# Performance work log

Measured on AMD Instinct MI355X. Metric: run time of the kernel, lower is better.

## Reference

```python
import jax, jax.numpy as jnp
import numpy as np

DIM = 128
WS = 7          # window size
NH = 4          # num heads
N = WS * WS     # tokens per window = 49
GRID = 56       # 224/4 token grid -> 8x8 = 64 windows per image
NUM_WIN = (GRID // WS) ** 2  # 64
IMG_B = 64
SCALE = (DIM // NH) ** -0.5


def _relative_position_index():
    coords = np.stack(np.meshgrid(np.arange(WS), np.arange(WS), indexing='ij'))  # (2,WS,WS)
    flat = coords.reshape(2, -1)                         # (2, N)
    rel = flat[:, :, None] - flat[:, None, :]            # (2, N, N)
    rel = rel.transpose(1, 2, 0).astype(np.int32)        # (N, N, 2)
    rel[:, :, 0] += WS - 1
    rel[:, :, 1] += WS - 1
    rel[:, :, 0] *= 2 * WS - 1
    return jnp.asarray(rel.sum(-1))                      # (N, N) int32


def _shift_mask():
    # Swin shifted-window attention mask: shift = WS // 2, off-group pairs get -100.
    shift = WS // 2
    img = np.zeros((GRID, GRID), dtype=np.int32)
    cnt = 0
    segs = (slice(0, -WS), slice(-WS, -shift), slice(-shift, None))
    for hs in segs:
        for ws_ in segs:
            img[hs, ws_] = cnt
            cnt += 1
    # window partition -> (NUM_WIN, N)
    w = img.reshape(GRID // WS, WS, GRID // WS, WS).transpose(0, 2, 1, 3).reshape(NUM_WIN, N)
    diff = w[:, :, None] - w[:, None, :]
    return jnp.asarray(np.where(diff != 0, -100.0, 0.0).astype(np.float32))  # (NUM_WIN, N, N)


def setup_inputs() -> dict:
    key = jax.random.key(0)
    ks = jax.random.split(key, 6)
    B = IMG_B * NUM_WIN  # 4096
    x = jax.random.normal(ks[0], (B, N, DIM), dtype=jnp.float32)
    qkv_w = jax.random.normal(ks[1], (3 * DIM, DIM), dtype=jnp.float32) * (DIM ** -0.5)
    qkv_b = jnp.zeros((3 * DIM,), dtype=jnp.float32)
    proj_w = jax.random.normal(ks[2], (DIM, DIM), dtype=jnp.float32) * (DIM ** -0.5)
    proj_b = jnp.zeros((DIM,), dtype=jnp.float32)
    rel_bias_table = jax.random.normal(ks[3], ((2 * WS - 1) ** 2, NH), dtype=jnp.float32) * 0.02
    return {
        'x': x,
        'mask': _shift_mask(),
        'qkv_w': qkv_w,
        'qkv_b': qkv_b,
        'proj_w': proj_w,
        'proj_b': proj_b,
        'rel_bias_table': rel_bias_table,
        'rel_index': _relative_position_index(),
    }


def reference(x, mask, qkv_w, qkv_b, proj_w, proj_b, rel_bias_table, rel_index):
    B, n, C = x.shape
    hd = C // NH
    qkv = (x @ qkv_w.T + qkv_b).reshape(B, n, 3, NH, hd)
    q = qkv[:, :, 0].transpose(0, 2, 1, 3) * SCALE   # (B, H, N, hd)
    k = qkv[:, :, 1].transpose(0, 2, 1, 3)
    v = qkv[:, :, 2].transpose(0, 2, 1, 3)
    attn = jnp.einsum('bhnd,bhmd->bhnm', q, k)       # (B, H, N, N)
    bias = rel_bias_table[rel_index.reshape(-1)].reshape(n, n, NH).transpose(2, 0, 1)
    attn = attn + bias[None]
    nW = mask.shape[0]
    attn = attn.reshape(B // nW, nW, NH, n, n) + mask[None, :, None]
    attn = jax.nn.softmax(attn.reshape(B, NH, n, n), axis=-1)
    out = jnp.einsum('bhnm,bhmd->bhnd', attn, v).transpose(0, 2, 1, 3).reshape(B, n, C)
    return out @ proj_w.T + proj_b
```

## Files before the change

### kernel.cpp

```cpp
#include <hip/hip_runtime.h>


#define NTOK  49
#define DIMC  128
#define NBLK  4096
#define SCALE 0.17677669529663687f

typedef __attribute__((ext_vector_type(8))) short bf16x8;
typedef __attribute__((ext_vector_type(4))) float f32x4;

#define WS_QKVW 0
#define WS_PROJW 49152
#define WS_BIAS  65536
#define WS_TOTAL 81920

#define XS_OFF 0
#define XS_STRIDE 136
#define PS_OFF 6664
#define PS_STRIDE 72
#define QS_OFF 10192
#define QS_STRIDE 40
#define KS_OFF 20432
#define VT_OFF 30672
#define VT_STRIDE 72
#define SMEM_TOT 39888

__device__ __forceinline__ unsigned int pkbf2(float f0, float f1) {
    union { float f; unsigned int i; } a, b; a.f = f0; b.f = f1;
    return __builtin_amdgcn_perm(b.i + 0x8000u, a.i + 0x8000u, 0x07060302u);
}
__device__ __forceinline__ unsigned short f2b_r(float f) {
    union { float f; unsigned int i; } v; v.f = f;
    return (unsigned short)((v.i + 0x8000u) >> 16);
}
__device__ __forceinline__ float b2f_lo(unsigned int u) {
    union { unsigned int i; float f; } v; v.i = u << 16; return v.f;
}
__device__ __forceinline__ float b2f_hi(unsigned int u) {
    union { unsigned int i; float f; } v; v.i = u & 0xFFFF0000u; return v.f;
}

__device__ __forceinline__ int seg3(int c) { return (c < 49) ? 0 : ((c < 53) ? 1 : 2); }

__global__ __launch_bounds__(256)
void prep(const float* __restrict__ qkv_w, const float* __restrict__ proj_w,
          const float* __restrict__ bias_t, const int* __restrict__ rel_idx,
          unsigned short* __restrict__ ws)
{
    int idx = blockIdx.x * 256 + threadIdx.x;
    if (idx < 8192) {
        int base = idx * 8;
        const float* sp = (base < 49152) ? (qkv_w + base) : (proj_w + (base - 49152));
        float sc = (base < 16384) ? SCALE : 1.0f;
        float4 a = *(const float4*)sp;
        float4 b = *(const float4*)(sp + 4);
        uint4 u;
        u.x = pkbf2(a.x * sc, a.y * sc);
        u.y = pkbf2(a.z * sc, a.w * sc);
        u.z = pkbf2(b.x * sc, b.y * sc);
        u.w = pkbf2(b.z * sc, b.w * sc);
        *(uint4*)(ws + base) = u;
    } else {
        int i = idx - 8192;
        int reg = i & 3, lane = (i >> 2) & 63, nt = (i >> 8) & 3,
            mt = (i >> 10) & 3, h = (i >> 12) & 3;
        int row = mt * 16 + (lane >> 4) * 4 + reg;
        int col = nt * 16 + (lane & 15);
        float v = 0.f;
        if (row < NTOK && col < NTOK)
            v = bias_t[rel_idx[row * NTOK + col] * 4 + h];
        ws[WS_BIAS + i] = f2b_r(v);
    }
}

__global__ __launch_bounds__(256, 2)
void win_attn(const float* __restrict__ x,
              const float* __restrict__ qkv_b,
              const float* __restrict__ proj_b,
              const unsigned short* __restrict__ ws,
              float* __restrict__ out)
{
    __shared__ unsigned short smem[SMEM_TOT];
    const int b    = blockIdx.x;
    const int w    = b & 63;
    const int tid  = threadIdx.x;
    const int wv   = tid >> 6;
    const int lane = tid & 63;
    const int qg   = lane >> 4;
    const int l15  = lane & 15;

    {
        const float4* xg = (const float4*)(x + (size_t)b * (NTOK * DIMC));
        for (int i = tid; i < NTOK * DIMC / 4; i += 256) {
            float4 v = xg[i];
            int row = i >> 5, col = (i & 31) * 4;
            uint2 u; u.x = pkbf2(v.x, v.y); u.y = pkbf2(v.z, v.w);
            *(uint2*)(smem + XS_OFF + row * XS_STRIDE + col) = u;
        }
    }
    __syncthreads();

    bf16x8 af[4][4];
    #pragma unroll
    for (int mt = 0; mt < 4; mt++) {
        int ar = mt * 16 + l15; if (ar > 48) ar = 48;
        #pragma unroll
        for (int ks_ = 0; ks_ < 4; ks_++)
            af[mt][ks_] = *(const bf16x8*)(smem + XS_OFF + ar * XS_STRIDE + ks_ * 32 + qg * 8);
    }

    {
        const unsigned short* qw = ws + WS_QKVW;
        #pragma unroll
        for (int part = 0; part < 3; part++) {
            #pragma unroll
            for (int half = 0; half < 2; half++) {
                const int jt = part * 8 + wv * 2 + half;
                const int j  = jt * 16 + l15;
                bf16x8 bf[4];
                #pragma unroll
                for (int ks_ = 0; ks_ < 4; ks_++)
                    bf[ks_] = *(const bf16x8*)(qw + j * DIMC + ks_ * 32 + qg * 8);
                const float bias = (part == 0) ? qkv_b[j] * SCALE : qkv_b[j];
                #pragma unroll
                for (int mt = 0; mt < 4; mt++) {
                    f32x4 acc = { bias, bias, bias, bias };
                    #pragma unroll
                    for (int ks_ = 0; ks_ < 4; ks_++)
                        acc = __builtin_amdgcn_mfma_f32_16x16x32_bf16(af[mt][ks_], bf[ks_], acc, 0, 0, 0);
                    const int d = half * 16 + l15;
                    if (part == 0) {
                        #pragma unroll
                        for (int r = 0; r < 4; r++) {
                            int row = mt * 16 + qg * 4 + r;
                            smem[QS_OFF + (wv * 64 + row) * QS_STRIDE + d] = f2b_r(acc[r]);
                        }
                    } else if (part == 1) {
                        #pragma unroll
                        for (int r = 0; r < 4; r++) {
                            int row = mt * 16 + qg * 4 + r;
                            smem[KS_OFF + (wv * 64 + row) * QS_STRIDE + d] = f2b_r(acc[r]);
                        }
                    } else {
                        uint2 u; u.x = pkbf2(acc[0], acc[1]); u.y = pkbf2(acc[2], acc[3]);
                        *(uint2*)(smem + VT_OFF + (wv * 32 + d) * VT_STRIDE + mt * 16 + qg * 4) = u;
                    }
                }
            }
        }
    }
    __syncthreads();

    const int wy = w >> 3, wx = w & 7;
    int g_row[4], g_col[4]; bool vcol[4];
    #pragma unroll
    for (int r = 0; r < 4; r++) {
        int t = wv * 16 + qg * 4 + r;
        int ty = (t * 9363) >> 16, tx = t - ty * 7;
        g_row[r] = seg3(wy * 7 + ty) * 3 + seg3(wx * 7 + tx);
    }
    #pragma unroll
    for (int nt = 0; nt < 4; nt++) {
        int t = nt * 16 + l15;
        int ty = (t * 9363) >> 16, tx = t - ty * 7;
        g_col[nt] = seg3(wy * 7 + ty) * 3 + seg3(wx * 7 + tx);
        vcol[nt] = t < NTOK;
    }

    const int r0 = wv * 16;
    for (int h = 0; h < 4; h++) {
        bf16x8 aq = *(const bf16x8*)(smem + QS_OFF + (h * 64 + r0 + l15) * QS_STRIDE + qg * 8);
        float s[4][4];
        #pragma unroll
        for (int nt = 0; nt < 4; nt++) {
            bf16x8 bk = *(const bf16x8*)(smem + KS_OFF + (h * 64 + nt * 16 + l15) * QS_STRIDE + qg * 8);
            f32x4 z = { 0.f, 0.f, 0.f, 0.f };
            f32x4 c = __builtin_amdgcn_mfma_f32_16x16x32_bf16(aq, bk, z, 0, 0, 0);
            uint2 bb = *(const uint2*)(ws + WS_BIAS + (((h * 4 + wv) * 4 + nt) * 64 + lane) * 4);
            float bv[4] = { b2f_lo(bb.x), b2f_hi(bb.x), b2f_lo(bb.y), b2f_hi(bb.y) };
            #pragma unroll
            for (int r = 0; r < 4; r++) {
                float v = c[r] + bv[r];
                v += (g_row[r] == g_col[nt]) ? 0.f : -100.f;
                s[nt][r] = vcol[nt] ? v : -1e30f;
            }
        }
        float p[4][4];
        #pragma unroll
        for (int r = 0; r < 4; r++) {
            float mx = fmaxf(fmaxf(s[0][r], s[1][r]), fmaxf(s[2][r], s[3][r]));
            mx = fmaxf(mx, __shfl_xor(mx, 1));
            mx = fmaxf(mx, __shfl_xor(mx, 2));
            mx = fmaxf(mx, __shfl_xor(mx, 4));
            mx = fmaxf(mx, __shfl_xor(mx, 8));
            float sum = 0.f;
            #pragma unroll
            for (int nt = 0; nt < 4; nt++) {
                float e = vcol[nt] ? __expf(s[nt][r] - mx) : 0.f;
                p[nt][r] = e; sum += e;
            }
            sum += __shfl_xor(sum, 1);
            sum += __shfl_xor(sum, 2);
            sum += __shfl_xor(sum, 4);
            sum += __shfl_xor(sum, 8);
            float inv = 1.f / sum;
            #pragma unroll
            for (int nt = 0; nt < 4; nt++) p[nt][r] *= inv;
        }
        #pragma unroll
        for (int nt = 0; nt < 4; nt++)
            #pragma unroll
            for (int r = 0; r < 4; r++) {
                int row = r0 + qg * 4 + r;
                if (row < NTOK)
                    smem[PS_OFF + row * PS_STRIDE + nt * 16 + l15] = f2b_r(p[nt][r]);
            }
        int ar2 = r0 + l15; if (ar2 > 48) ar2 = 48;
        f32x4 accO[2] = { { 0.f, 0.f, 0.f, 0.f }, { 0.f, 0.f, 0.f, 0.f } };
        #pragma unroll
        for (int ks2 = 0; ks2 < 2; ks2++) {
            bf16x8 ap = *(const bf16x8*)(smem + PS_OFF + ar2 * PS_STRIDE + ks2 * 32 + qg * 8);
            #pragma unroll
            for (int nt2 = 0; nt2 < 2; nt2++) {
                bf16x8 bv = *(const bf16x8*)(smem + VT_OFF + (h * 32 + nt2 * 16 + l15) * VT_STRIDE + ks2 * 32 + qg * 8);
                accO[nt2] = __builtin_amdgcn_mfma_f32_16x16x32_bf16(ap, bv, accO[nt2], 0, 0, 0);
            }
        }
        #pragma unroll
        for (int nt2 = 0; nt2 < 2; nt2++)
            #pragma unroll
            for (int r = 0; r < 4; r++) {
                int row = r0 + qg * 4 + r;
                if (row < NTOK)
                    smem[XS_OFF + row * XS_STRIDE + h * 32 + nt2 * 16 + l15] = f2b_r(accO[nt2][r]);
            }
    }
    __syncthreads();

    {
        #pragma unroll
        for (int mt = 0; mt < 4; mt++) {
            int ar = mt * 16 + l15; if (ar > 48) ar = 48;
            #pragma unroll
            for (int ks_ = 0; ks_ < 4; ks_++)
                af[mt][ks_] = *(const bf16x8*)(smem + XS_OFF + ar * XS_STRIDE + ks_ * 32 + qg * 8);
        }
        const unsigned short* pw = ws + WS_PROJW;
        float* ob = out + (size_t)b * (NTOK * DIMC);
        #pragma unroll
        for (int half = 0; half < 2; half++) {
            const int j = (wv * 2 + half) * 16 + l15;
            bf16x8 bf[4];
            #pragma unroll
            for (int ks_ = 0; ks_ < 4; ks_++)
                bf[ks_] = *(const bf16x8*)(pw + j * DIMC + ks_ * 32 + qg * 8);
            const float pb = proj_b[j];
            #pragma unroll
            for (int mt = 0; mt < 4; mt++) {
                f32x4 acc = { pb, pb, pb, pb };
                #pragma unroll
                for (int ks_ = 0; ks_ < 4; ks_++)
                    acc = __builtin_amdgcn_mfma_f32_16x16x32_bf16(af[mt][ks_], bf[ks_], acc, 0, 0, 0);
                #pragma unroll
                for (int r = 0; r < 4; r++) {
                    int row = mt * 16 + qg * 4 + r;
                    if (row < NTOK) ob[row * DIMC + j] = acc[r];
                }
            }
        }
    }
}

extern "C" void kernel_launch(void* const* d_in, const int* in_sizes, int n_in,
                              void* d_out, int out_size, void* d_ws, size_t ws_size,
                              hipStream_t stream) {
    const float* x      = (const float*)d_in[0];
    const float* qkv_w  = (const float*)d_in[2];
    const float* qkv_b  = (const float*)d_in[3];
    const float* proj_w = (const float*)d_in[4];
    const float* proj_b = (const float*)d_in[5];
    const float* bias_t = (const float*)d_in[6];
    const int*   relidx = (const int*)d_in[7];
    float*       outp   = (float*)d_out;
    unsigned short* ws  = (unsigned short*)d_ws;

    prep<<<96, 256, 0, stream>>>(qkv_w, proj_w, bias_t, relidx, ws);
    win_attn<<<NBLK, 256, 0, stream>>>(x, qkv_b, proj_b, ws, outp);
}
```

Baseline: 299.2 us.

## Use 512-thread blocks with head-split attention, exp2 softmax, and compact LDS

```diff
diff --git a/kernel.cpp b/kernel.cpp
--- a/kernel.cpp
+++ b/kernel.cpp
@@ -5,6 +5,8 @@
 #define DIMC  128
 #define NBLK  4096
 #define SCALE 0.17677669529663687f
+#define LOG2E 1.4426950408889634f
+#define NMASK -144.26950408889634f
 
 typedef __attribute__((ext_vector_type(8))) short bf16x8;
 typedef __attribute__((ext_vector_type(4))) float f32x4;
@@ -14,16 +16,17 @@
 #define WS_BIAS  65536
 #define WS_TOTAL 81920
 
-#define XS_OFF 0
+#define PS_OFF    0
+#define PS_G      3528
+#define PS_STRIDE 72
 #define XS_STRIDE 136
-#define PS_OFF 6664
-#define PS_STRIDE 72
-#define QS_OFF 10192
+#define QS_OFF    7056
+#define QS_HB     2080
 #define QS_STRIDE 40
-#define KS_OFF 20432
-#define VT_OFF 30672
+#define KS_OFF    15376
+#define VT_OFF    23696
 #define VT_STRIDE 72
-#define SMEM_TOT 39888
+#define SMEM_TOT  32912
 
 __device__ __forceinline__ unsigned int pkbf2(float f0, float f1) {
     union { float f; unsigned int i; } a, b; a.f = f0; b.f = f1;
@@ -38,6 +41,9 @@
 }
 __device__ __forceinline__ float b2f_hi(unsigned int u) {
     union { unsigned int i; float f; } v; v.i = u & 0xFFFF0000u; return v.f;
+}
+__device__ __forceinline__ float exp2_hw(float x) {
+    float r; asm("v_exp_f32 %0, %1" : "=v"(r) : "v"(x)); return r;
 }
 
 __device__ __forceinline__ int seg3(int c) { return (c < 49) ? 0 : ((c < 53) ? 1 : 2); }
@@ -51,7 +57,7 @@
     if (idx < 8192) {
         int base = idx * 8;
         const float* sp = (base < 49152) ? (qkv_w + base) : (proj_w + (base - 49152));
-        float sc = (base < 16384) ? SCALE : 1.0f;
+        float sc = (base < 16384) ? (SCALE * LOG2E) : 1.0f;
         float4 a = *(const float4*)sp;
         float4 b = *(const float4*)(sp + 4);
         uint4 u;
@@ -68,12 +74,12 @@
         int col = nt * 16 + (lane & 15);
         float v = 0.f;
         if (row < NTOK && col < NTOK)
-            v = bias_t[rel_idx[row * NTOK + col] * 4 + h];
+            v = bias_t[rel_idx[row * NTOK + col] * 4 + h] * LOG2E;
         ws[WS_BIAS + i] = f2b_r(v);
     }
 }
 
-__global__ __launch_bounds__(256, 2)
+__global__ __launch_bounds__(512, 4)
 void win_attn(const float* __restrict__ x,
               const float* __restrict__ qkv_b,
               const float* __restrict__ proj_b,
@@ -91,11 +97,22 @@
 
     {
         const float4* xg = (const float4*)(x + (size_t)b * (NTOK * DIMC));
-        for (int i = tid; i < NTOK * DIMC / 4; i += 256) {
-            float4 v = xg[i];
-            int row = i >> 5, col = (i & 31) * 4;
-            uint2 u; u.x = pkbf2(v.x, v.y); u.y = pkbf2(v.z, v.w);
-            *(uint2*)(smem + XS_OFF + row * XS_STRIDE + col) = u;
+        #pragma unroll
+        for (int it = 0; it < 4; it++) {
+            int i = tid + it * 512;
+            if (i < NTOK * DIMC / 4) {
+                float4 v = xg[i];
+                int row = i >> 5, col = (i & 31) * 4;
+                uint2 u; u.x = pkbf2(v.x, v.y); u.y = pkbf2(v.z, v.w);
+                *(uint2*)(smem + PS_OFF + row * XS_STRIDE + col) = u;
+            }
+        }
+        if (tid < 384) {
+            int hz = tid / 96;
+            int rem = tid - hz * 96;
+            int rowz = NTOK + (rem >> 5);
+            int dz = rem & 31;
+            smem[KS_OFF + hz * QS_HB + rowz * QS_STRIDE + dz] = 0;
         }
     }
     __syncthreads();
@@ -106,89 +123,96 @@
         int ar = mt * 16 + l15; if (ar > 48) ar = 48;
         #pragma unroll
         for (int ks_ = 0; ks_ < 4; ks_++)
-            af[mt][ks_] = *(const bf16x8*)(smem + XS_OFF + ar * XS_STRIDE + ks_ * 32 + qg * 8);
+            af[mt][ks_] = *(const bf16x8*)(smem + PS_OFF + ar * XS_STRIDE + ks_ * 32 + qg * 8);
     }
 
     {
         const unsigned short* qw = ws + WS_QKVW;
-        #pragma unroll
-        for (int part = 0; part < 3; part++) {
-            #pragma unroll
-            for (int half = 0; half < 2; half++) {
-                const int jt = part * 8 + wv * 2 + half;
-                const int j  = jt * 16 + l15;
-                bf16x8 bf[4];
+        const int h2 = wv >> 1;
+        const int dh = (wv & 1) * 16 + l15;
+        #pragma unroll
+        for (int pp = 0; pp < 3; pp++) {
+            const int j = (pp * 8 + wv) * 16 + l15;
+            bf16x8 bfr[4];
+            #pragma unroll
+            for (int ks_ = 0; ks_ < 4; ks_++)
+                bfr[ks_] = *(const bf16x8*)(qw + j * DIMC + ks_ * 32 + qg * 8);
+            const float bias = (pp == 0) ? qkv_b[j] * (SCALE * LOG2E) : qkv_b[j];
+            #pragma unroll
+            for (int mt = 0; mt < 4; mt++) {
+                f32x4 acc = { bias, bias, bias, bias };
                 #pragma unroll
                 for (int ks_ = 0; ks_ < 4; ks_++)
-                    bf[ks_] = *(const bf16x8*)(qw + j * DIMC + ks_ * 32 + qg * 8);
-                const float bias = (part == 0) ? qkv_b[j] * SCALE : qkv_b[j];
-                #pragma unroll
-                for (int mt = 0; mt < 4; mt++) {
-                    f32x4 acc = { bias, bias, bias, bias };
+                    acc = __builtin_amdgcn_mfma_f32_16x16x32_bf16(af[mt][ks_], bfr[ks_], acc, 0, 0, 0);
+                if (pp == 0) {
                     #pragma unroll
-                    for (int ks_ = 0; ks_ < 4; ks_++)
-                        acc = __builtin_amdgcn_mfma_f32_16x16x32_bf16(af[mt][ks_], bf[ks_], acc, 0, 0, 0);
-                    const int d = half * 16 + l15;
-                    if (part == 0) {
-                        #pragma unroll
-                        for (int r = 0; r < 4; r++) {
-                            int row = mt * 16 + qg * 4 + r;
-                            smem[QS_OFF + (wv * 64 + row) * QS_STRIDE + d] = f2b_r(acc[r]);
-                        }
-                    } else if (part == 1) {
-                        #pragma unroll
-                        for (int r = 0; r < 4; r++) {
-                            int row = mt * 16 + qg * 4 + r;
-                            smem[KS_OFF + (wv * 64 + row) * QS_STRIDE + d] = f2b_r(acc[r]);
-                        }
-                    } else {
-                        uint2 u; u.x = pkbf2(acc[0], acc[1]); u.y = pkbf2(acc[2], acc[3]);
-                        *(uint2*)(smem + VT_OFF + (wv * 32 + d) * VT_STRIDE + mt * 16 + qg * 4) = u;
+                    for (int r = 0; r < 4; r++) {
+                        int row = mt * 16 + qg * 4 + r;
+                        if (row < NTOK)
+                            smem[QS_OFF + h2 * QS_HB + row * QS_STRIDE + dh] = f2b_r(acc[r]);
                     }
+                } else if (pp == 1) {
+                    #pragma unroll
+                    for (int r = 0; r < 4; r++) {
+                        int row = mt * 16 + qg * 4 + r;
+                        if (row < NTOK)
+                            smem[KS_OFF + h2 * QS_HB + row * QS_STRIDE + dh] = f2b_r(acc[r]);
+                    }
+                } else {
+                    uint2 u; u.x = pkbf2(acc[0], acc[1]); u.y = pkbf2(acc[2], acc[3]);
+                    *(uint2*)(smem + VT_OFF + (h2 * 32 + dh) * VT_STRIDE + mt * 16 + qg * 4) = u;
                 }
             }
         }
     }
     __syncthreads();
 
+    const int g  = wv >> 2;
+    const int st = wv & 3;
+    const int r0 = st * 16;
     const int wy = w >> 3, wx = w & 7;
-    int g_row[4], g_col[4]; bool vcol[4];
+    float mreg[4][4];
+    {
+        int grow[4];
+        #pragma unroll
+        for (int r = 0; r < 4; r++) {
+            int t = r0 + qg * 4 + r;
+            int ty = (t * 9363) >> 16, tx = t - ty * 7;
+            grow[r] = seg3(wy * 7 + ty) * 3 + seg3(wx * 7 + tx);
+        }
+        #pragma unroll
+        for (int nt = 0; nt < 4; nt++) {
+            int t = nt * 16 + l15;
+            int ty = (t * 9363) >> 16, tx = t - ty * 7;
+            int gcol = seg3(wy * 7 + ty) * 3 + seg3(wx * 7 + tx);
+            bool vc = t < NTOK;
+            #pragma unroll
+            for (int r = 0; r < 4; r++)
+                mreg[nt][r] = !vc ? -1e30f : ((grow[r] == gcol) ? 0.f : NMASK);
+        }
+    }
+    int ar2 = r0 + l15; if (ar2 > 48) ar2 = 48;
+
     #pragma unroll
-    for (int r = 0; r < 4; r++) {
-        int t = wv * 16 + qg * 4 + r;
-        int ty = (t * 9363) >> 16, tx = t - ty * 7;
-        g_row[r] = seg3(wy * 7 + ty) * 3 + seg3(wx * 7 + tx);
-    }
-    #pragma unroll
-    for (int nt = 0; nt < 4; nt++) {
-        int t = nt * 16 + l15;
-        int ty = (t * 9363) >> 16, tx = t - ty * 7;
-        g_col[nt] = seg3(wy * 7 + ty) * 3 + seg3(wx * 7 + tx);
-        vcol[nt] = t < NTOK;
-    }
-
-    const int r0 = wv * 16;
-    for (int h = 0; h < 4; h++) {
-        bf16x8 aq = *(const bf16x8*)(smem + QS_OFF + (h * 64 + r0 + l15) * QS_STRIDE + qg * 8);
-        float s[4][4];
+    for (int hh = 0; hh < 2; hh++) {
+        const int h = g * 2 + hh;
+        const bf16x8 aq = *(const bf16x8*)(smem + QS_OFF + h * QS_HB + ar2 * QS_STRIDE + qg * 8);
+        float sv[4][4];
         #pragma unroll
         for (int nt = 0; nt < 4; nt++) {
-            bf16x8 bk = *(const bf16x8*)(smem + KS_OFF + (h * 64 + nt * 16 + l15) * QS_STRIDE + qg * 8);
+            bf16x8 bk = *(const bf16x8*)(smem + KS_OFF + h * QS_HB + (nt * 16 + l15) * QS_STRIDE + qg * 8);
             f32x4 z = { 0.f, 0.f, 0.f, 0.f };
             f32x4 c = __builtin_amdgcn_mfma_f32_16x16x32_bf16(aq, bk, z, 0, 0, 0);
-            uint2 bb = *(const uint2*)(ws + WS_BIAS + (((h * 4 + wv) * 4 + nt) * 64 + lane) * 4);
-            float bv[4] = { b2f_lo(bb.x), b2f_hi(bb.x), b2f_lo(bb.y), b2f_hi(bb.y) };
-            #pragma unroll
-            for (int r = 0; r < 4; r++) {
-                float v = c[r] + bv[r];
-                v += (g_row[r] == g_col[nt]) ? 0.f : -100.f;
-                s[nt][r] = vcol[nt] ? v : -1e30f;
-            }
-        }
-        float p[4][4];
+            uint2 bb = *(const uint2*)(ws + WS_BIAS + (((h * 4 + st) * 4 + nt) * 64 + lane) * 4);
+            sv[nt][0] = c[0] + b2f_lo(bb.x) + mreg[nt][0];
+            sv[nt][1] = c[1] + b2f_hi(bb.x) + mreg[nt][1];
+            sv[nt][2] = c[2] + b2f_lo(bb.y) + mreg[nt][2];
+            sv[nt][3] = c[3] + b2f_hi(bb.y) + mreg[nt][3];
+        }
+        float p[4][4], inv[4];
         #pragma unroll
         for (int r = 0; r < 4; r++) {
-            float mx = fmaxf(fmaxf(s[0][r], s[1][r]), fmaxf(s[2][r], s[3][r]));
+            float mx = fmaxf(fmaxf(sv[0][r], sv[1][r]), fmaxf(sv[2][r], sv[3][r]));
             mx = fmaxf(mx, __shfl_xor(mx, 1));
             mx = fmaxf(mx, __shfl_xor(mx, 2));
             mx = fmaxf(mx, __shfl_xor(mx, 4));
@@ -196,16 +220,14 @@
             float sum = 0.f;
             #pragma unroll
             for (int nt = 0; nt < 4; nt++) {
-                float e = vcol[nt] ? __expf(s[nt][r] - mx) : 0.f;
+                float e = exp2_hw(sv[nt][r] - mx);
                 p[nt][r] = e; sum += e;
             }
             sum += __shfl_xor(sum, 1);
             sum += __shfl_xor(sum, 2);
             sum += __shfl_xor(sum, 4);
             sum += __shfl_xor(sum, 8);
-            float inv = 1.f / sum;
-            #pragma unroll
-            for (int nt = 0; nt < 4; nt++) p[nt][r] *= inv;
+            inv[r] = __builtin_amdgcn_rcpf(sum);
         }
         #pragma unroll
         for (int nt = 0; nt < 4; nt++)
@@ -213,17 +235,16 @@
             for (int r = 0; r < 4; r++) {
                 int row = r0 + qg * 4 + r;
                 if (row < NTOK)
-                    smem[PS_OFF + row * PS_STRIDE + nt * 16 + l15] = f2b_r(p[nt][r]);
-            }
-        int ar2 = r0 + l15; if (ar2 > 48) ar2 = 48;
+                    smem[PS_OFF + g * PS_G + row * PS_STRIDE + nt * 16 + l15] = f2b_r(p[nt][r]);
+            }
         f32x4 accO[2] = { { 0.f, 0.f, 0.f, 0.f }, { 0.f, 0.f, 0.f, 0.f } };
         #pragma unroll
         for (int ks2 = 0; ks2 < 2; ks2++) {
-            bf16x8 ap = *(const bf16x8*)(smem + PS_OFF + ar2 * PS_STRIDE + ks2 * 32 + qg * 8);
+            bf16x8 ap = *(const bf16x8*)(smem + PS_OFF + g * PS_G + ar2 * PS_STRIDE + ks2 * 32 + qg * 8);
             #pragma unroll
             for (int nt2 = 0; nt2 < 2; nt2++) {
-                bf16x8 bv = *(const bf16x8*)(smem + VT_OFF + (h * 32 + nt2 * 16 + l15) * VT_STRIDE + ks2 * 32 + qg * 8);
-                accO[nt2] = __builtin_amdgcn_mfma_f32_16x16x32_bf16(ap, bv, accO[nt2], 0, 0, 0);
+                bf16x8 bvv = *(const bf16x8*)(smem + VT_OFF + (h * 32 + nt2 * 16 + l15) * VT_STRIDE + ks2 * 32 + qg * 8);
+                accO[nt2] = __builtin_amdgcn_mfma_f32_16x16x32_bf16(ap, bvv, accO[nt2], 0, 0, 0);
             }
         }
         #pragma unroll
@@ -232,40 +253,37 @@
             for (int r = 0; r < 4; r++) {
                 int row = r0 + qg * 4 + r;
                 if (row < NTOK)
-                    smem[XS_OFF + row * XS_STRIDE + h * 32 + nt2 * 16 + l15] = f2b_r(accO[nt2][r]);
+                    smem[QS_OFF + h * QS_HB + row * QS_STRIDE + nt2 * 16 + l15] =
+                        f2b_r(accO[nt2][r] * inv[r]);
             }
     }
     __syncthreads();
 
     {
-        #pragma unroll
-        for (int mt = 0; mt < 4; mt++) {
-            int ar = mt * 16 + l15; if (ar > 48) ar = 48;
-            #pragma unroll
-            for (int ks_ = 0; ks_ < 4; ks_++)
-                af[mt][ks_] = *(const bf16x8*)(smem + XS_OFF + ar * XS_STRIDE + ks_ * 32 + qg * 8);
-        }
+        const int mt = wv & 3, jh = wv >> 2;
+        int ar = mt * 16 + l15; if (ar > 48) ar = 48;
+        bf16x8 ad[4];
+        #pragma unroll
+        for (int ks_ = 0; ks_ < 4; ks_++)
+            ad[ks_] = *(const bf16x8*)(smem + QS_OFF + ks_ * QS_HB + ar * QS_STRIDE + qg * 8);
         const unsigned short* pw = ws + WS_PROJW;
         float* ob = out + (size_t)b * (NTOK * DIMC);
         #pragma unroll
-        for (int half = 0; half < 2; half++) {
-            const int j = (wv * 2 + half) * 16 + l15;
-            bf16x8 bf[4];
+        for (int jt2 = 0; jt2 < 4; jt2++) {
+            const int j = jh * 64 + jt2 * 16 + l15;
+            bf16x8 bfr[4];
             #pragma unroll
             for (int ks_ = 0; ks_ < 4; ks_++)
-                bf[ks_] = *(const bf16x8*)(pw + j * DIMC + ks_ * 32 + qg * 8);
+                bfr[ks_] = *(const bf16x8*)(pw + j * DIMC + ks_ * 32 + qg * 8);
             const float pb = proj_b[j];
-            #pragma unroll
-            for (int mt = 0; mt < 4; mt++) {
-                f32x4 acc = { pb, pb, pb, pb };
-                #pragma unroll
-                for (int ks_ = 0; ks_ < 4; ks_++)
-                    acc = __builtin_amdgcn_mfma_f32_16x16x32_bf16(af[mt][ks_], bf[ks_], acc, 0, 0, 0);
-                #pragma unroll
-                for (int r = 0; r < 4; r++) {
-                    int row = mt * 16 + qg * 4 + r;
-                    if (row < NTOK) ob[row * DIMC + j] = acc[r];
-                }
+            f32x4 acc = { pb, pb, pb, pb };
+            #pragma unroll
+            for (int ks_ = 0; ks_ < 4; ks_++)
+                acc = __builtin_amdgcn_mfma_f32_16x16x32_bf16(ad[ks_], bfr[ks_], acc, 0, 0, 0);
+            #pragma unroll
+            for (int r = 0; r < 4; r++) {
+                int row = mt * 16 + qg * 4 + r;
+                if (row < NTOK) ob[row * DIMC + j] = acc[r];
             }
         }
     }
@@ -285,5 +303,5 @@
     unsigned short* ws  = (unsigned short*)d_ws;
 
     prep<<<96, 256, 0, stream>>>(qkv_w, proj_w, bias_t, relidx, ws);
-    win_attn<<<NBLK, 256, 0, stream>>>(x, qkv_b, proj_b, ws, outp);
-}
+    win_attn<<<NBLK, 512, 0, stream>>>(x, qkv_b, proj_b, ws, outp);
+}
```

After: 300.6 us. Within noise of the previous version (+0.5%).
